# Optimization experiments

Measured on AMD Instinct MI355X. Metric: run time of the kernel, lower is better.

The kernel has to match this reference:

```python
import jax, jax.numpy as jnp
import numpy as np

N = 4096        # num nodes
D = 512         # d_model (in_dim)
F = 512         # dff (out_dim)
H = 4           # num_heads
ALPHA = 0.3     # tf.keras LeakyReLU default


def setup_inputs() -> dict:
    key = jax.random.key(0)
    ks = jax.random.split(key, 9)
    s_in = 1.0 / np.sqrt(D)
    s_out = 1.0 / np.sqrt(F)
    return {
        "nodes": jax.random.normal(ks[0], (N, D), jnp.float32),
        "edges": jax.random.normal(ks[1], (N, D), jnp.float32),
        "labels": jax.random.normal(ks[2], (N, D), jnp.float32),
        # edge_layer Dense(dff)
        "We": jax.random.normal(ks[3], (D, F), jnp.float32) * s_in,
        "be": jnp.zeros((F,), jnp.float32),
        # per-head kernels stacked on leading head axis
        "W": jax.random.normal(ks[4], (H, D, F), jnp.float32) * s_in,
        "b": jax.random.normal(ks[5], (H, F), jnp.float32) * 0.01,
        "u": jax.random.normal(ks[6], (H, F), jnp.float32) * s_out,  # attn_kernel_self (squeezed)
        "v": jax.random.normal(ks[7], (H, F), jnp.float32) * s_out,  # attn_kernel_neighs (squeezed)
    }


def reference(nodes, edges, labels, We, be, W, b, u, v):
    # edge projection shared across heads: Dense(edges + labels)
    e = (edges + labels) @ We + be                       # [N, F]
    # per-head node projection: features = nodes @ W_h + b_h
    feats = jnp.einsum('nd,hdf->hnf', nodes, W) + b[:, None, :]   # [H, N, F]
    # rank-1 additive attention scores
    a_self = jnp.einsum('hnf,hf->hn', feats, u)          # [H, N]
    a_neigh = jnp.einsum('hnf,hf->hn', feats, v)         # [H, N]
    feats = feats + e[None]                              # [H, N, F]
    scores = a_self[:, :, None] * a_neigh[:, None, :]    # [H, N, N] outer product
    scores = jnp.where(scores >= 0, scores, ALPHA * scores)  # LeakyReLU(0.3)
    attn = jax.nn.softmax(scores, axis=-1)               # [H, N, N]
    out = jnp.einsum('hnm,hmf->hnf', attn, feats)        # [H, N, F]
    return jax.nn.relu(out.mean(axis=0))                 # [N, F]
```

## Files before the change

### kernel.cpp

```cpp
#include <hip/hip_runtime.h>

#define NN 4096
#define DD 512
#define FF 512
#define HH 4
#define KK 1024

typedef _Float16 f16;
typedef f16 f16x8 __attribute__((ext_vector_type(8)));
typedef f16 f16x4 __attribute__((ext_vector_type(4)));
typedef float f32x4 __attribute__((ext_vector_type(4)));
typedef float f32x16 __attribute__((ext_vector_type(16)));

typedef __attribute__((address_space(1))) void gvoid;
typedef __attribute__((address_space(3))) void svoid;
__device__ __forceinline__ void glds16(const void* g, void* s) {
    __builtin_amdgcn_global_load_lds((gvoid*)g, (svoid*)s, 16, 0, 0);
}

__device__ __attribute__((aligned(16))) f16 g_catA[NN * KK];
__device__ __attribute__((aligned(16))) f16 g_catB[HH * FF * KK];
__device__ __attribute__((aligned(16))) f16 g_featsH[HH * FF * NN];
__device__ __attribute__((aligned(16))) f16 g_oaccH[(size_t)2 * HH * NN * FF];
__device__ float g_Zp[2 * HH * NN];
__device__ float g_bcat[HH * FF];
__device__ float g_tu[HH * DD], g_tv[HH * DD], g_bu[HH], g_bv[HH];
__device__ float g_p[HH * NN], g_q[HH * NN];

#define PREP_CONV 4104
#define PREP_TRAN 320
#define PREP_UV   513

__global__ __launch_bounds__(256) void k_prep(const float* __restrict__ nodes, const float* __restrict__ edges,
                                              const float* __restrict__ labels, const float* __restrict__ We,
                                              const float* __restrict__ W, const float* __restrict__ be,
                                              const float* __restrict__ b, const float* __restrict__ u,
                                              const float* __restrict__ v) {
    __shared__ float lds[64 * 65];
    int bx = blockIdx.x;
    int tid = threadIdx.x;
    if (bx < PREP_CONV) {
        int id = bx * 256 + tid;
        const int NQ = NN * DD / 4;
        if (id < NQ) {
            f32x4 vv = *(const f32x4*)(nodes + (size_t)id * 4);
            f16x4 ov;
#pragma unroll
            for (int k = 0; k < 4; ++k) ov[k] = (f16)vv[k];
            *(f16x4*)&g_catA[(size_t)(id >> 7) * KK + (id & 127) * 4] = ov;
            return;
        }
        id -= NQ;
        if (id < NQ) {
            f32x4 ev = *(const f32x4*)(edges  + (size_t)id * 4);
            f32x4 lv = *(const f32x4*)(labels + (size_t)id * 4);
            f16x4 ov;
#pragma unroll
            for (int k = 0; k < 4; ++k) ov[k] = (f16)(ev[k] + lv[k]);
            *(f16x4*)&g_catA[(size_t)(id >> 7) * KK + 512 + (id & 127) * 4] = ov;
            return;
        }
        id -= NQ;
        if (id < HH * FF) { g_bcat[id] = b[id] + be[id & 511]; return; }
        return;
    }
    if (bx < PREP_CONV + PREP_TRAN) {
        int bid = bx - PREP_CONV;
        int mi = bid >> 6;
        int t64 = bid & 63;
        const float* src = (mi == 0) ? We : (W + (size_t)(mi - 1) * DD * FF);
        int ti = t64 >> 3, tj = t64 & 7;
        int r = tid >> 2, cseg = (tid & 3) * 16;
#pragma unroll
        for (int kq = 0; kq < 4; ++kq) {
            f32x4 vv = *(const f32x4*)(src + (size_t)(ti * 64 + r) * 512 + tj * 64 + cseg + kq * 4);
            *(f32x4*)&lds[r * 65 + cseg + kq * 4] = vv;
        }
        __syncthreads();
        int fl = tid >> 2, dseg = (tid & 3) * 16;
        f16x8 o0, o1;
#pragma unroll
        for (int k = 0; k < 8; ++k) o0[k] = (f16)lds[(dseg + k) * 65 + fl];
#pragma unroll
        for (int k = 0; k < 8; ++k) o1[k] = (f16)lds[(dseg + 8 + k) * 65 + fl];
        size_t frow = (size_t)(tj * 64 + fl);
        size_t dcol = (size_t)(ti * 64 + dseg);
        if (mi == 0) {
#pragma unroll
            for (int hh = 0; hh < HH; ++hh) {
                size_t ob = ((size_t)hh * FF + frow) * KK + 512 + dcol;
                *(f16x8*)&g_catB[ob] = o0;
                *(f16x8*)&g_catB[ob + 8] = o1;
            }
        } else {
            size_t ob = ((size_t)(mi - 1) * FF + frow) * KK + dcol;
            *(f16x8*)&g_catB[ob] = o0;
            *(f16x8*)&g_catB[ob + 8] = o1;
        }
        return;
    }
    {
        int row = (bx - PREP_CONV - PREP_TRAN) * 4 + (tid >> 6);
        int lane = tid & 63;
        float su = 0.f, sv = 0.f;
        if (row < HH * DD) {
            int h = row >> 9, d = row & 511;
            size_t wb = (size_t)h * DD * FF + (size_t)d * FF;
#pragma unroll
            for (int j = 0; j < 8; ++j) {
                int f = lane + 64 * j;
                float wv = W[wb + f];
                su += wv * u[(size_t)h * FF + f];
                sv += wv * v[(size_t)h * FF + f];
            }
        } else if (row < HH * DD + HH) {
            int h = row - HH * DD;
#pragma unroll
            for (int j = 0; j < 8; ++j) {
                int f = lane + 64 * j;
                float bvv = b[(size_t)h * FF + f];
                su += bvv * u[(size_t)h * FF + f];
                sv += bvv * v[(size_t)h * FF + f];
            }
        }
#pragma unroll
        for (int m = 1; m < 64; m <<= 1) {
            su += __shfl_xor(su, m, 64);
            sv += __shfl_xor(sv, m, 64);
        }
        if (lane == 0 && row < HH * DD + HH) {
            if (row < HH * DD) { g_tu[row] = su; g_tv[row] = sv; }
            else { g_bu[row - HH * DD] = su; g_bv[row - HH * DD] = sv; }
        }
    }
}

__global__ __launch_bounds__(256, 2) void k_feats_pq() {
    __shared__ f16 As[128 * 128];
    __shared__ f16 Bs[128 * 128];
    int tid = threadIdx.x;
    int bid = blockIdx.x;
    if (bid >= 512) {
        int row = (bid - 512) * 4 + (tid >> 6);
        int lane = tid & 63;
        int h = row >> 12, n = row & 4095;
        const f16* nb = g_catA + (size_t)n * KK + lane * 8;
        const float* tu = g_tu + h * DD + lane * 8;
        const float* tv = g_tv + h * DD + lane * 8;
        f16x8 nv8 = *(const f16x8*)nb;
        f32x4 tu0 = *(const f32x4*)tu, tu1 = *(const f32x4*)(tu + 4);
        f32x4 tv0 = *(const f32x4*)tv, tv1 = *(const f32x4*)(tv + 4);
        float pa = 0.f, qa = 0.f;
#pragma unroll
        for (int j = 0; j < 4; ++j) {
            float nv = (float)nv8[j];
            pa += nv * tu0[j];
            qa += nv * tv0[j];
        }
#pragma unroll
        for (int j = 0; j < 4; ++j) {
            float nv = (float)nv8[4 + j];
            pa += nv * tu1[j];
            qa += nv * tv1[j];
        }
#pragma unroll
        for (int m = 1; m < 64; m <<= 1) {
            pa += __shfl_xor(pa, m, 64);
            qa += __shfl_xor(qa, m, 64);
        }
        if (lane == 0) {
            g_p[row] = pa + g_bu[h];
            g_q[row] = qa + g_bv[h];
        }
        return;
    }
    int lane = tid & 63, wave = tid >> 6;
    int wr = wave & 1, wc = wave >> 1;
    int c5 = lane & 31, h5 = lane >> 5;
    int n0 = (bid & 31) * 128, f0 = ((bid >> 5) & 3) * 128;
    int h = bid >> 7;
    const f16* Bgl = g_catB + (size_t)h * FF * KK;
    int r4 = lane >> 4;
    int ch = lane & 15;
    f32x16 acc[2][2] = {};
    int ra0 = wr * 64 + c5, ra1 = ra0 + 32;
    int rb0 = wc * 64 + c5, rb1 = rb0 + 32;
    for (int kk = 0; kk < KK; kk += 128) {
        __syncthreads();
#pragma unroll
        for (int j = 0; j < 8; ++j) {
            int rowb = wave * 32 + j * 4;
            int row = rowb + r4;
            int src = (ch ^ (row & 15)) * 8;
            glds16(g_catA + (size_t)(n0 + row) * KK + kk + src, &As[rowb * 128]);
            glds16(Bgl    + (size_t)(f0 + row) * KK + kk + src, &Bs[rowb * 128]);
        }
        __syncthreads();
#pragma unroll
        for (int sk = 0; sk < 8; ++sk) {
            int lc = sk * 2 + h5;
            f16x8 af0 = *(const f16x8*)&As[ra0 * 128 + ((lc ^ (ra0 & 15)) * 8)];
            f16x8 af1 = *(const f16x8*)&As[ra1 * 128 + ((lc ^ (ra1 & 15)) * 8)];
            f16x8 bf0 = *(const f16x8*)&Bs[rb0 * 128 + ((lc ^ (rb0 & 15)) * 8)];
            f16x8 bf1 = *(const f16x8*)&Bs[rb1 * 128 + ((lc ^ (rb1 & 15)) * 8)];
            acc[0][0] = __builtin_amdgcn_mfma_f32_32x32x16_f16(af0, bf0, acc[0][0], 0, 0, 0);
            acc[0][1] = __builtin_amdgcn_mfma_f32_32x32x16_f16(af0, bf1, acc[0][1], 0, 0, 0);
            acc[1][0] = __builtin_amdgcn_mfma_f32_32x32x16_f16(af1, bf0, acc[1][0], 0, 0, 0);
            acc[1][1] = __builtin_amdgcn_mfma_f32_32x32x16_f16(af1, bf1, acc[1][1], 0, 0, 0);
        }
    }
#pragma unroll
    for (int it = 0; it < 2; ++it)
#pragma unroll
        for (int jt = 0; jt < 2; ++jt) {
            int f = f0 + wc * 64 + jt * 32 + c5;
            float bv = g_bcat[h * FF + f];
#pragma unroll
            for (int qd = 0; qd < 4; ++qd) {
                int r0 = n0 + wr * 64 + it * 32 + qd * 8 + h5 * 4;
                f16x4 ov;
#pragma unroll
                for (int rr = 0; rr < 4; ++rr) ov[rr] = (f16)(acc[it][jt][qd * 4 + rr] + bv);
                *(f16x4*)(g_featsH + ((size_t)h * FF + f) * NN + r0) = ov;
            }
        }
}

#define WCALC(qv, dstvec, idx)                                              \
    {                                                                       \
        float s_ = pv * (qv);                                               \
        s_ = fmaxf(s_, 0.3f * s_);                                          \
        float e_ = __builtin_amdgcn_exp2f(__builtin_fmaf(s_, L2E, -mvb));   \
        zacc += e_;                                                         \
        dstvec[idx] = (f16)e_;                                              \
    }
#define GEN8(qa, qb, w)                                                     \
    {                                                                       \
        _Pragma("unroll") for (int k_ = 0; k_ < 4; ++k_) {                  \
            WCALC((qa)[k_], w, k_);                                         \
            WCALC((qb)[k_], w, 4 + k_);                                     \
        }                                                                   \
    }
#define STAGE_B(buf, kkoff)                                                 \
    {                                                                       \
        _Pragma("unroll") for (int j = 0; j < 8; ++j) {                     \
            int row_ = wave * 64 + j * 8 + r8;                              \
            glds16(Bgl + (size_t)row_ * NN + (kkoff) + ((ch ^ (row_ & 7)) * 8), \
                   &Bs[buf][(wave * 64 + j * 8) * 64]);                     \
        }                                                                   \
    }

__global__ __launch_bounds__(512, 2) void k_gemm_out() {
    __shared__ f16 As2[2][128 * 64];
    __shared__ f16 Bs[2][512 * 64];
    int tid = threadIdx.x;
    int lane = tid & 63, wave = tid >> 6;
    int wr = wave & 1;
    int wf = wave >> 1;
    int c5 = lane & 31, h5 = lane >> 5;
    int n0 = blockIdx.x * 128;
    int h = blockIdx.y;
    int ks = blockIdx.z;
    int wn = tid >> 2, kq = (tid & 3) * 16;
    const float L2E = 1.44269504f;
    float pv = g_p[h * NN + n0 + wn];
    const float* qh = g_q + h * NN + ks * 2048;
    const f16* Bgl = g_featsH + (size_t)h * FF * NN + (size_t)ks * 2048;
    int r8 = lane >> 3, ch = lane & 7;
    float mvb;
    {
        const float* qfull = g_q + h * NN + tid * 8;
        f32x4 a = *(const f32x4*)qfull, b2 = *(const f32x4*)(qfull + 4);
        float lmax = -1e30f, lmin = 1e30f;
#pragma unroll
        for (int j = 0; j < 4; ++j) {
            lmax = fmaxf(lmax, fmaxf(a[j], b2[j]));
            lmin = fminf(lmin, fminf(a[j], b2[j]));
        }
#pragma unroll
        for (int m = 1; m < 64; m <<= 1) {
            lmax = fmaxf(lmax, __shfl_xor(lmax, m, 64));
            lmin = fminf(lmin, __shfl_xor(lmin, m, 64));
        }
        float* red = (float*)&As2[0][0];
        if (lane == 0) { red[wave] = lmax; red[8 + wave] = lmin; }
        __syncthreads();
        float qmax = red[0], qmin = red[8];
#pragma unroll
        for (int w2 = 1; w2 < 8; ++w2) {
            qmax = fmaxf(qmax, red[w2]);
            qmin = fminf(qmin, red[8 + w2]);
        }
        float se = pv * (pv >= 0.f ? qmax : qmin);
        float Mv = fmaxf(se, 0.3f * se);
        mvb = Mv * L2E + 6.0f;
        __syncthreads();
    }
    int aw0 = wn * 64 + (((tid & 3) * 2 + 0) ^ (wn & 7)) * 8;
    int aw1 = wn * 64 + (((tid & 3) * 2 + 1) ^ (wn & 7)) * 8;
    int arow = (wr * 64 + c5) * 64;
    int brow = (wf * 128 + c5) * 64;
    int csw = (c5 & 7);
    float zacc = 0.f;
    f32x16 acc[2][4] = {};
    f16x8 wA, wB;

    {
        const float* qp = qh + kq;
        f32x4 q0 = *(const f32x4*)qp, q1 = *(const f32x4*)(qp + 4),
              q2 = *(const f32x4*)(qp + 8), q3 = *(const f32x4*)(qp + 12);
        GEN8(q0, q1, wA);
        GEN8(q2, q3, wB);
        *(f16x8*)&As2[0][aw0] = wA;
        *(f16x8*)&As2[0][aw1] = wB;
        STAGE_B(0, 0);
        const float* qp1 = qh + 64 + kq;
        q0 = *(const f32x4*)qp1; q1 = *(const f32x4*)(qp1 + 4);
        q2 = *(const f32x4*)(qp1 + 8); q3 = *(const f32x4*)(qp1 + 12);
        GEN8(q0, q1, wA);
        GEN8(q2, q3, wB);
    }
    __syncthreads();

    int cur = 0;
    for (int t = 0; t < 32; ++t) {
        f32x4 q0, q1, q2, q3;
        if (t < 30) {
            const float* qp = qh + t * 64 + 128 + kq;
            q0 = *(const f32x4*)qp; q1 = *(const f32x4*)(qp + 4);
            q2 = *(const f32x4*)(qp + 8); q3 = *(const f32x4*)(qp + 12);
        }
        if (t < 31) {
            int nxt = cur ^ 1;
            int kk2 = t * 64 + 64;
            STAGE_B(nxt, kk2);
            *(f16x8*)&As2[nxt][aw0] = wA;
            *(f16x8*)&As2[nxt][aw1] = wB;
        }
#pragma unroll
        for (int sk = 0; sk < 4; ++sk) {
            int cph = ((sk * 2 + h5) ^ csw) * 8;
            f16x8 af0 = *(const f16x8*)&As2[cur][arow + cph];
            f16x8 af1 = *(const f16x8*)&As2[cur][arow + 2048 + cph];
            f16x8 bf0 = *(const f16x8*)&Bs[cur][brow + cph];
            f16x8 bf1 = *(const f16x8*)&Bs[cur][brow + 2048 + cph];
            f16x8 bf2 = *(const f16x8*)&Bs[cur][brow + 4096 + cph];
            f16x8 bf3 = *(const f16x8*)&Bs[cur][brow + 6144 + cph];
            acc[0][0] = __builtin_amdgcn_mfma_f32_32x32x16_f16(af0, bf0, acc[0][0], 0, 0, 0);
            acc[0][1] = __builtin_amdgcn_mfma_f32_32x32x16_f16(af0, bf1, acc[0][1], 0, 0, 0);
            acc[0][2] = __builtin_amdgcn_mfma_f32_32x32x16_f16(af0, bf2, acc[0][2], 0, 0, 0);
            acc[0][3] = __builtin_amdgcn_mfma_f32_32x32x16_f16(af0, bf3, acc[0][3], 0, 0, 0);
            acc[1][0] = __builtin_amdgcn_mfma_f32_32x32x16_f16(af1, bf0, acc[1][0], 0, 0, 0);
            acc[1][1] = __builtin_amdgcn_mfma_f32_32x32x16_f16(af1, bf1, acc[1][1], 0, 0, 0);
            acc[1][2] = __builtin_amdgcn_mfma_f32_32x32x16_f16(af1, bf2, acc[1][2], 0, 0, 0);
            acc[1][3] = __builtin_amdgcn_mfma_f32_32x32x16_f16(af1, bf3, acc[1][3], 0, 0, 0);
            if (t < 30) {
                if (sk == 1) { GEN8(q0, q1, wA); }
                if (sk == 2) { GEN8(q2, q3, wB); }
            }
        }
        __syncthreads();
        cur ^= 1;
    }
    zacc += __shfl_xor(zacc, 1, 64);
    zacc += __shfl_xor(zacc, 2, 64);
    if ((tid & 3) == 0) g_Zp[(size_t)(h * 2 + ks) * NN + n0 + wn] = zacc;
    f16* O = g_oaccH + (size_t)(h * 2 + ks) * NN * FF;
#pragma unroll
    for (int it = 0; it < 2; ++it)
#pragma unroll
        for (int jt = 0; jt < 4; ++jt) {
            int f = wf * 128 + jt * 32 + c5;
#pragma unroll
            for (int qd = 0; qd < 4; ++qd) {
                int r0 = n0 + wr * 64 + it * 32 + qd * 8 + h5 * 4;
#pragma unroll
                for (int rr = 0; rr < 4; ++rr)
                    O[(size_t)(r0 + rr) * FF + f] = (f16)acc[it][jt][qd * 4 + rr];
            }
        }
}

__global__ void k_reduce(float* __restrict__ out) {
    int t = blockIdx.x * 256 + threadIdx.x;
    size_t i = (size_t)t * 8;
    int n = t >> 6;
    const size_t NF = (size_t)NN * FF;
    float s[8] = {0.f, 0.f, 0.f, 0.f, 0.f, 0.f, 0.f, 0.f};
#pragma unroll
    for (int h = 0; h < HH; ++h) {
        float Z = g_Zp[(size_t)(2 * h) * NN + n] + g_Zp[(size_t)(2 * h + 1) * NN + n];
        float sc = 0.25f / Z;
        f16x8 a = *(const f16x8*)(g_oaccH + (size_t)(2 * h) * NF + i);
        f16x8 bsl = *(const f16x8*)(g_oaccH + (size_t)(2 * h + 1) * NF + i);
#pragma unroll
        for (int rr = 0; rr < 8; ++rr) s[rr] += ((float)a[rr] + (float)bsl[rr]) * sc;
    }
    f32x4 o0, o1;
#pragma unroll
    for (int rr = 0; rr < 4; ++rr) o0[rr] = fmaxf(s[rr], 0.f);
#pragma unroll
    for (int rr = 0; rr < 4; ++rr) o1[rr] = fmaxf(s[4 + rr], 0.f);
    *(f32x4*)(out + i) = o0;
    *(f32x4*)(out + i + 4) = o1;
}

extern "C" void kernel_launch(void* const* d_in, const int* in_sizes, int n_in,
                              void* d_out, int out_size, void* d_ws, size_t ws_size,
                              hipStream_t stream) {
    (void)in_sizes; (void)n_in; (void)out_size; (void)d_ws; (void)ws_size;
    const float* nodes  = (const float*)d_in[0];
    const float* edges  = (const float*)d_in[1];
    const float* labels = (const float*)d_in[2];
    const float* We     = (const float*)d_in[3];
    const float* be     = (const float*)d_in[4];
    const float* W      = (const float*)d_in[5];
    const float* b      = (const float*)d_in[6];
    const float* u      = (const float*)d_in[7];
    const float* v      = (const float*)d_in[8];

    k_prep<<<PREP_CONV + PREP_TRAN + PREP_UV, 256, 0, stream>>>(nodes, edges, labels, We, W, be, b, u, v);
    k_feats_pq<<<512 + 4096, 256, 0, stream>>>();
    k_gemm_out<<<dim3(32, 4, 2), 512, 0, stream>>>();
    k_reduce<<<1024, 256, 0, stream>>>((float*)d_out);
}
```

Before: 218.2 us.

## Compute shared edge projection once instead of per head in feats GEMM

The per-head feats GEMM previously ran over a concatenated K of 1024 (nodes plus edges+labels), recomputing the head-independent edge projection for every head. A separate GEMM now computes e once into a transposed fp16 buffer, and the per-head GEMM runs over K=512 only, adding e and the head bias in the epilogue. This halves the MFMA work of the feats stage at the cost of an extra kernel launch, an extra fp16 round trip of e, and a slightly different rounding order.

```diff
diff --git a/kernel.cpp b/kernel.cpp
--- a/kernel.cpp
+++ b/kernel.cpp
@@ -20,6 +20,7 @@
 
 __device__ __attribute__((aligned(16))) f16 g_catA[NN * KK];
 __device__ __attribute__((aligned(16))) f16 g_catB[HH * FF * KK];
+__device__ __attribute__((aligned(16))) f16 g_eT[(size_t)FF * NN];
 __device__ __attribute__((aligned(16))) f16 g_featsH[HH * FF * NN];
 __device__ __attribute__((aligned(16))) f16 g_oaccH[(size_t)2 * HH * NN * FF];
 __device__ float g_Zp[2 * HH * NN];
@@ -135,7 +136,63 @@
     }
 }
 
-__global__ __launch_bounds__(256, 2) void k_feats_pq() {
+__global__ __launch_bounds__(256, 2) void k_egemm(const float* __restrict__ be) {
+    __shared__ f16 As[128 * 128];
+    __shared__ f16 Bs[128 * 128];
+    int tid = threadIdx.x;
+    int lane = tid & 63, wave = tid >> 6;
+    int wr = wave & 1, wc = wave >> 1;
+    int c5 = lane & 31, h5 = lane >> 5;
+    int n0 = blockIdx.x * 128, f0 = blockIdx.y * 128;
+    const f16* Agl = g_catA + 512;
+    const f16* Bgl = g_catB + 512;
+    int r4 = lane >> 4;
+    int ch = lane & 15;
+    f32x16 acc[2][2] = {};
+    int ra0 = wr * 64 + c5, ra1 = ra0 + 32;
+    int rb0 = wc * 64 + c5, rb1 = rb0 + 32;
+    for (int kk = 0; kk < 512; kk += 128) {
+        __syncthreads();
+#pragma unroll
+        for (int j = 0; j < 8; ++j) {
+            int rowb = wave * 32 + j * 4;
+            int row = rowb + r4;
+            int src = (ch ^ (row & 15)) * 8;
+            glds16(Agl + (size_t)(n0 + row) * KK + kk + src, &As[rowb * 128]);
+            glds16(Bgl + (size_t)(f0 + row) * KK + kk + src, &Bs[rowb * 128]);
+        }
+        __syncthreads();
+#pragma unroll
+        for (int sk = 0; sk < 8; ++sk) {
+            int lc = sk * 2 + h5;
+            f16x8 af0 = *(const f16x8*)&As[ra0 * 128 + ((lc ^ (ra0 & 15)) * 8)];
+            f16x8 af1 = *(const f16x8*)&As[ra1 * 128 + ((lc ^ (ra1 & 15)) * 8)];
+            f16x8 bf0 = *(const f16x8*)&Bs[rb0 * 128 + ((lc ^ (rb0 & 15)) * 8)];
+            f16x8 bf1 = *(const f16x8*)&Bs[rb1 * 128 + ((lc ^ (rb1 & 15)) * 8)];
+            acc[0][0] = __builtin_amdgcn_mfma_f32_32x32x16_f16(af0, bf0, acc[0][0], 0, 0, 0);
+            acc[0][1] = __builtin_amdgcn_mfma_f32_32x32x16_f16(af0, bf1, acc[0][1], 0, 0, 0);
+            acc[1][0] = __builtin_amdgcn_mfma_f32_32x32x16_f16(af1, bf0, acc[1][0], 0, 0, 0);
+            acc[1][1] = __builtin_amdgcn_mfma_f32_32x32x16_f16(af1, bf1, acc[1][1], 0, 0, 0);
+        }
+    }
+#pragma unroll
+    for (int it = 0; it < 2; ++it)
+#pragma unroll
+        for (int jt = 0; jt < 2; ++jt) {
+            int f = f0 + wc * 64 + jt * 32 + c5;
+            float bv = be[f];
+#pragma unroll
+            for (int qd = 0; qd < 4; ++qd) {
+                int r0 = n0 + wr * 64 + it * 32 + qd * 8 + h5 * 4;
+                f16x4 ov;
+#pragma unroll
+                for (int rr = 0; rr < 4; ++rr) ov[rr] = (f16)(acc[it][jt][qd * 4 + rr] + bv);
+                *(f16x4*)(g_eT + (size_t)f * NN + r0) = ov;
+            }
+        }
+}
+
+__global__ __launch_bounds__(256, 2) void k_feats_pq(const float* __restrict__ b) {
     __shared__ f16 As[128 * 128];
     __shared__ f16 Bs[128 * 128];
     int tid = threadIdx.x;
@@ -185,7 +242,7 @@
     f32x16 acc[2][2] = {};
     int ra0 = wr * 64 + c5, ra1 = ra0 + 32;
     int rb0 = wc * 64 + c5, rb1 = rb0 + 32;
-    for (int kk = 0; kk < KK; kk += 128) {
+    for (int kk = 0; kk < 512; kk += 128) {
         __syncthreads();
 #pragma unroll
         for (int j = 0; j < 8; ++j) {
@@ -214,13 +271,15 @@
 #pragma unroll
         for (int jt = 0; jt < 2; ++jt) {
             int f = f0 + wc * 64 + jt * 32 + c5;
-            float bv = g_bcat[h * FF + f];
+            float bv = b[(size_t)h * FF + f];
 #pragma unroll
             for (int qd = 0; qd < 4; ++qd) {
                 int r0 = n0 + wr * 64 + it * 32 + qd * 8 + h5 * 4;
+                f16x4 ev = *(const f16x4*)(g_eT + (size_t)f * NN + r0);
                 f16x4 ov;
 #pragma unroll
-                for (int rr = 0; rr < 4; ++rr) ov[rr] = (f16)(acc[it][jt][qd * 4 + rr] + bv);
+                for (int rr = 0; rr < 4; ++rr)
+                    ov[rr] = (f16)(acc[it][jt][qd * 4 + rr] + bv + (float)ev[rr]);
                 *(f16x4*)(g_featsH + ((size_t)h * FF + f) * NN + r0) = ov;
             }
         }
@@ -420,7 +479,8 @@
     const float* v      = (const float*)d_in[8];
 
     k_prep<<<PREP_CONV + PREP_TRAN + PREP_UV, 256, 0, stream>>>(nodes, edges, labels, We, W, be, b, u, v);
-    k_feats_pq<<<512 + 4096, 256, 0, stream>>>();
+    k_egemm<<<dim3(32, 4), 256, 0, stream>>>(be);
+    k_feats_pq<<<512 + 4096, 256, 0, stream>>>(b);
     k_gemm_out<<<dim3(32, 4, 2), 512, 0, stream>>>();
     k_reduce<<<1024, 256, 0, stream>>>((float*)d_out);
 }
```

Measured after the change: 224.5 us. 2.9% more time.
